# Kernel optimization log

Hardware: AMD Instinct MI355X
Metric: run time of the kernel (lower is better)

The kernel has to match this reference:

```python
import jax, jax.numpy as jnp
import numpy as np

BN_EPS = 1e-5


def _binary_activation(x):
    # forward value = sign(x); gradient flows through piecewise poly o3 (STE)
    s = jnp.sign(x)
    o1 = jnp.where(x < -1.0, -1.0, x * x + 2.0 * x)
    o2 = jnp.where(x < 0.0, o1, -x * x + 2.0 * x)
    o3 = jnp.where(x < 1.0, o2, 1.0)
    return jax.lax.stop_gradient(s - o3) + o3


def _binarize_weights(w):
    # sign_function: fwd 2*(w>0)-1, bwd identity (STE)
    sgn = 2.0 * (w > 0.0).astype(w.dtype) - 1.0
    wb = jax.lax.stop_gradient(sgn - w) + w
    # detached per-output-channel scale: mean |w| over (in, kh, kw)
    scale = jax.lax.stop_gradient(jnp.mean(jnp.abs(w), axis=(1, 2, 3), keepdims=True))
    return scale * wb


def setup_inputs() -> dict:
    key = jax.random.key(0)
    k1, k2, k3 = jax.random.split(key, 3)
    C = 64
    x = jax.random.normal(k1, (32, C, 112, 112), dtype=jnp.float32)
    w = jax.random.uniform(k2, (C, C, 3, 3), dtype=jnp.float32) * 0.001
    return {
        "x": x,
        "b0": jnp.zeros((1, C, 1, 1), jnp.float32),
        "w": w,
        "gamma": jnp.ones((C,), jnp.float32),
        "beta": jnp.zeros((C,), jnp.float32),
        "b1": jnp.zeros((1, C, 1, 1), jnp.float32),
        "alpha": jnp.full((C,), 0.25, jnp.float32),  # PReLU default init
        "b2": jnp.zeros((1, C, 1, 1), jnp.float32),
    }


def reference(x, b0, w, gamma, beta, b1, alpha, b2):
    residual = x
    out = x + b0                       # move0
    out = _binary_activation(out)      # binary activation
    bw = _binarize_weights(w)
    out = jax.lax.conv_general_dilated(
        out, bw, window_strides=(1, 1), padding=[(1, 1), (1, 1)],
        dimension_numbers=("NCHW", "OIHW", "NCHW"))
    # BatchNorm2d in training mode (batch stats, biased variance)
    mu = jnp.mean(out, axis=(0, 2, 3), keepdims=True)
    var = jnp.var(out, axis=(0, 2, 3), keepdims=True)
    g = gamma.reshape(1, -1, 1, 1)
    b = beta.reshape(1, -1, 1, 1)
    out = (out - mu) * jax.lax.rsqrt(var + BN_EPS) * g + b
    out = out + residual
    out = out + b1                     # move1
    a = alpha.reshape(1, -1, 1, 1)
    out = jnp.where(out > 0, out, a * out)  # PReLU
    out = out + b2                     # move2
    return out
```

## Files before the change

### kernel.cpp

```cpp
#include <hip/hip_runtime.h>
#include <stdint.h>

#define C 64
#define HH 112
#define WWD 112
#define HW 12544
#define NB 32
#define MTOT (NB*HW)
#define PLANE_SH 25088
#define PLANE_BYTES 50176
#define ROWB 7168
#define HOLE_OFF 25088

typedef int v4i  __attribute__((ext_vector_type(4)));
typedef int v16i __attribute__((ext_vector_type(16)));
typedef unsigned long long ull;

__device__ __forceinline__ const char* sign_row_c(const char* outb, int R) {
    return outb + (size_t)(R/3)*PLANE_BYTES + HOLE_OFF + (size_t)(R%3)*ROWB;
}
__device__ __forceinline__ char* sign_row(char* outb, int R) {
    return outb + (size_t)(R/3)*PLANE_BYTES + HOLE_OFF + (size_t)(R%3)*ROWB;
}

__global__ __launch_bounds__(256) void k_pack(
        const float* __restrict__ x, const float* __restrict__ b0,
        const float* __restrict__ w,
        char* __restrict__ outb, char* __restrict__ A8, float* __restrict__ wscale) {
    int bid = blockIdx.x;
    if (bid < 1568) {
        __shared__ ull Tl[256*9];
        int tid = threadIdx.x;
        int n    = bid / 49;
        int pimg = (bid % 49) * 256 + tid;
        const float* xb = x + (size_t)n*C*HW + pimg;
        ull row[8];
        #pragma unroll
        for (int k = 0; k < 8; ++k) {
            ull r = 0;
            #pragma unroll
            for (int j = 0; j < 8; ++j) {
                int c = k*8 + j;
                float v = xb[(size_t)c*HW] + b0[c];
                int sg = v > 0.f ? 1 : (v < 0.f ? 0xFF : 0);
                r |= ((ull)(unsigned)sg) << (8*j);
            }
            row[k] = r;
        }
        #pragma unroll
        for (int k = 0; k < 8; ++k) Tl[tid*9 + k] = row[k];
        __syncthreads();
        int wv = tid >> 6, L = tid & 63;
        #pragma unroll
        for (int j = 0; j < 4; ++j) {
            int prow = wv*64 + j*16 + (L >> 2);
            int cch  = L & 3;
            ull a0 = Tl[prow*9 + cch*2];
            ull a1 = Tl[prow*9 + cch*2 + 1];
            int pb = (bid % 49)*256 + wv*64 + j*16;
            int hg = pb / WWD;
            int wg = pb - hg*WWD;
            char* dst = sign_row(outb, n*HH + hg) + wg*64 + (size_t)L*16;
            uint4 val;
            val.x = (uint32_t)a0; val.y = (uint32_t)(a0 >> 32);
            val.z = (uint32_t)a1; val.w = (uint32_t)(a1 >> 32);
            *(uint4*)dst = val;
        }
    } else {
        int t = threadIdx.x;
        int o = t >> 2, part = t & 3;
        float s = 0.f;
        for (int cc = 0; cc < 16; ++cc) {
            int c = part*16 + cc;
            const float* wp = w + ((size_t)o*C + c)*9;
            #pragma unroll
            for (int tap = 0; tap < 9; ++tap) {
                float v = wp[tap];
                s += fabsf(v);
                A8[(o*9 + tap)*64 + c] = v > 0.f ? (char)1 : (char)-1;
            }
        }
        __shared__ float pabs[256];
        pabs[t] = s;
        __syncthreads();
        if (t < 64)
            wscale[t] = (pabs[t*4]+pabs[t*4+1]+pabs[t*4+2]+pabs[t*4+3]) * (1.0f/576.0f);
    }
}

__global__ __launch_bounds__(256) void k_conv(
        const char* __restrict__ signb, const char* __restrict__ A8,
        short* __restrict__ cv16) {
    __shared__ ull ldsq[4*114*9];
    int n  = blockIdx.y;
    int rb = blockIdx.x * 2;

    for (int it = threadIdx.x; it < 4*448; it += 256) {
        int ri = it / 448;
        int k  = it - ri*448;
        int col = k >> 2;
        int b   = k & 3;
        int Rr = rb - 1 + ri;
        uint4 v = make_uint4(0,0,0,0);
        if (Rr >= 0 && Rr < HH)
            v = ((const uint4*)sign_row_c(signb, n*HH + Rr))[k];
        ull* d = &ldsq[((size_t)(ri*114 + col + 1))*9 + b*2];
        d[0] = ((ull)v.y << 32) | v.x;
        d[1] = ((ull)v.w << 32) | v.z;
    }
    if (threadIdx.x < 72) {
        int r = threadIdx.x / 18, rest = threadIdx.x % 18;
        int col = (rest / 9) * 113, q = rest % 9;
        ldsq[((size_t)(r*114 + col))*9 + q] = 0ull;
    }

    int lane  = threadIdx.x & 63;
    int wv    = threadIdx.x >> 6;
    int ot    = wv & 1;
    int gsel  = lane >> 5;
    int olane = ot*32 + (lane & 31);

    v4i afr[9][2];
    #pragma unroll
    for (int tap = 0; tap < 9; ++tap) {
        #pragma unroll
        for (int h = 0; h < 2; ++h)
            afr[tap][h] = *(const v4i*)(A8 + (size_t)(olane*9 + tap)*64 + h*32 + gsel*16);
    }
    __syncthreads();

    for (int T = (wv >> 1); T < 7; T += 2) {
        int px   = T*32 + (lane & 31);
        int roff = px >= WWD ? 1 : 0;
        int cpx  = px - roff*WWD;
        v16i accA = {0,0,0,0,0,0,0,0,0,0,0,0,0,0,0,0};
        v16i accB = {0,0,0,0,0,0,0,0,0,0,0,0,0,0,0,0};
        #pragma unroll
        for (int kh = 0; kh < 3; ++kh) {
            #pragma unroll
            for (int kw = 0; kw < 3; ++kw) {
                const ull* bp = &ldsq[((size_t)((roff+kh)*114 + (cpx+kw)))*9];
                ull lo0 = bp[gsel*2],     hi0 = bp[gsel*2 + 1];
                ull lo1 = bp[gsel*2 + 4], hi1 = bp[gsel*2 + 5];
                v4i b0v = {(int)lo0, (int)(lo0>>32), (int)hi0, (int)(hi0>>32)};
                v4i b1v = {(int)lo1, (int)(lo1>>32), (int)hi1, (int)(hi1>>32)};
                accA = __builtin_amdgcn_mfma_i32_32x32x32_i8(afr[kh*3+kw][0], b0v, accA, 0, 0, 0);
                accB = __builtin_amdgcn_mfma_i32_32x32x32_i8(afr[kh*3+kw][1], b1v, accB, 0, 0, 0);
            }
        }
        v16i acc = accA + accB;
        size_t pixbase = (size_t)rb*WWD + px;
        #pragma unroll
        for (int r = 0; r < 16; ++r) {
            int o = ot*32 + (r & 3) + 8*(r >> 2) + 4*gsel;
            cv16[(size_t)(n*C + o)*PLANE_SH + pixbase] = (short)acc[r];
        }
    }
}

__global__ __launch_bounds__(256) void k_stats(
        const short* __restrict__ cv16, int* __restrict__ ps,
        long long* __restrict__ pq) {
    int plane = blockIdx.x;
    const uint2* p = (const uint2*)(cv16 + (size_t)plane*PLANE_SH);
    int s = 0; unsigned q = 0;
    for (int i = threadIdx.x; i < 3136; i += 256) {
        uint2 u = p[i];
        int v0 = (int)(short)(u.x & 0xFFFF), v1 = (int)(short)(u.x >> 16);
        int v2 = (int)(short)(u.y & 0xFFFF), v3 = (int)(short)(u.y >> 16);
        s += (v0+v1) + (v2+v3);
        q += (unsigned)(v0*v0 + v1*v1) + (unsigned)(v2*v2 + v3*v3);
    }
    __shared__ int ls[256];
    __shared__ unsigned long long lq[256];
    ls[threadIdx.x] = s; lq[threadIdx.x] = q;
    __syncthreads();
    for (int st = 128; st > 0; st >>= 1) {
        if ((int)threadIdx.x < st) {
            ls[threadIdx.x] += ls[threadIdx.x+st];
            lq[threadIdx.x] += lq[threadIdx.x+st];
        }
        __syncthreads();
    }
    if (threadIdx.x == 0) { ps[plane] = ls[0]; pq[plane] = (long long)lq[0]; }
}

__global__ __launch_bounds__(256) void k_finish(
        const short* __restrict__ cv16, const float* __restrict__ x,
        const int* __restrict__ ps, const long long* __restrict__ pq,
        const float* __restrict__ wscale, const float* __restrict__ gamma,
        const float* __restrict__ beta, const float* __restrict__ b1,
        const float* __restrict__ alpha, const float* __restrict__ b2,
        float* __restrict__ out) {
    int o = blockIdx.x, n = blockIdx.y;
    size_t plane = (size_t)n*C + o;

    int s = 0; long long q = 0;
    #pragma unroll 8
    for (int nn = 0; nn < NB; ++nn) { s += ps[nn*C + o]; q += pq[nn*C + o]; }
    const float inv = 1.0f / (float)MTOT;
    float sc   = wscale[o];
    float mean = (float)s * inv;
    float ek2  = (float)q * inv;
    float mu   = sc * mean;
    float var  = sc*sc*ek2 - mu*mu;
    float g    = gamma[o] * rsqrtf(var + 1e-5f);
    float A    = g * sc;
    float B    = beta[o] - g*mu + b1[o];
    float al   = alpha[o];
    float bb2  = b2[o];

    const uint2* cv2 = (const uint2*)(cv16 + plane*PLANE_SH);
    uint2 rbuf[13];
    #pragma unroll
    for (int k = 0; k < 13; ++k) {
        int i = threadIdx.x + k*256;
        if (i < 3136) rbuf[k] = cv2[i];
    }
    __syncthreads();

    const float4* x4 = (const float4*)x + plane*3136;
    float4*       o4 = (float4*)out     + plane*3136;
    #pragma unroll
    for (int k = 0; k < 13; ++k) {
        int i = threadIdx.x + k*256;
        if (i < 3136) {
            uint2 u = rbuf[k];
            float4 xv = x4[i], r;
            float t;
            t = A * (float)(int)(short)(u.x & 0xFFFF) + B + xv.x; t = t > 0.f ? t : al*t; r.x = t + bb2;
            t = A * (float)(int)(short)(u.x >> 16)    + B + xv.y; t = t > 0.f ? t : al*t; r.y = t + bb2;
            t = A * (float)(int)(short)(u.y & 0xFFFF) + B + xv.z; t = t > 0.f ? t : al*t; r.z = t + bb2;
            t = A * (float)(int)(short)(u.y >> 16)    + B + xv.w; t = t > 0.f ? t : al*t; r.w = t + bb2;
            o4[i] = r;
        }
    }
}

extern "C" void kernel_launch(void* const* d_in, const int* in_sizes, int n_in,
                              void* d_out, int out_size, void* d_ws, size_t ws_size,
                              hipStream_t stream) {
    const float* x     = (const float*)d_in[0];
    const float* b0    = (const float*)d_in[1];
    const float* w     = (const float*)d_in[2];
    const float* gamma = (const float*)d_in[3];
    const float* beta  = (const float*)d_in[4];
    const float* b1    = (const float*)d_in[5];
    const float* alpha = (const float*)d_in[6];
    const float* b2    = (const float*)d_in[7];

    char* ws = (char*)d_ws;
    char*      A8     = ws;
    float*     wscale = (float*)(ws + 36864);
    int*       ps     = (int*)(ws + 37120);
    long long* pq     = (long long*)(ws + 45312);

    char*  outb = (char*)d_out;
    short* cv16 = (short*)d_out;

    hipLaunchKernelGGL(k_pack, dim3(1569), dim3(256), 0, stream,
                       x, b0, w, outb, A8, wscale);
    hipLaunchKernelGGL(k_conv, dim3(56, 32), dim3(256), 0, stream,
                       outb, A8, cv16);
    hipLaunchKernelGGL(k_stats, dim3(2048), dim3(256), 0, stream,
                       cv16, ps, pq);
    hipLaunchKernelGGL(k_finish, dim3(64, 32), dim3(256), 0, stream,
                       cv16, x, ps, pq, wscale, gamma, beta, b1, alpha, b2,
                       (float*)d_out);
}
```

Baseline: 120.5 us.

## Fuse activation sign-packing into conv kernel, drop packed intermediate buffer

Removes the separate pack pass that wrote channel-interleaved sign bytes into the output buffer. The conv kernel now reads fp32 x rows directly, computes sign bytes, and transposes them to channel-minor layout with lane shuffles and byte permutes before storing to LDS. Weight prep moves to its own single-block kernel. This avoids a global write and read of the packed sign tensor and one pass over it. In exchange, each input row is loaded as fp32 by two neighbouring row-blocks (halo rows), and the conv prologue does more ALU and shuffle work.

```diff
diff --git a/kernel.cpp b/kernel.cpp
--- a/kernel.cpp
+++ b/kernel.cpp
@@ -8,115 +8,87 @@
 #define NB 32
 #define MTOT (NB*HW)
 #define PLANE_SH 25088
-#define PLANE_BYTES 50176
-#define ROWB 7168
-#define HOLE_OFF 25088
 
 typedef int v4i  __attribute__((ext_vector_type(4)));
 typedef int v16i __attribute__((ext_vector_type(16)));
 typedef unsigned long long ull;
 
-__device__ __forceinline__ const char* sign_row_c(const char* outb, int R) {
-    return outb + (size_t)(R/3)*PLANE_BYTES + HOLE_OFF + (size_t)(R%3)*ROWB;
-}
-__device__ __forceinline__ char* sign_row(char* outb, int R) {
-    return outb + (size_t)(R/3)*PLANE_BYTES + HOLE_OFF + (size_t)(R%3)*ROWB;
-}
-
-__global__ __launch_bounds__(256) void k_pack(
+__device__ __forceinline__ uint32_t sgn_byte(float v) {
+    return v > 0.f ? 1u : (v < 0.f ? 0xFFu : 0u);
+}
+
+__global__ __launch_bounds__(256) void k_wprep(
+        const float* __restrict__ w, char* __restrict__ A8,
+        float* __restrict__ wscale) {
+    int t = threadIdx.x;
+    int o = t >> 2, part = t & 3;
+    float s = 0.f;
+    for (int cc = 0; cc < 16; ++cc) {
+        int c = part*16 + cc;
+        const float* wp = w + ((size_t)o*C + c)*9;
+        #pragma unroll
+        for (int tap = 0; tap < 9; ++tap) {
+            float v = wp[tap];
+            s += fabsf(v);
+            A8[(o*9 + tap)*64 + c] = v > 0.f ? (char)1 : (char)-1;
+        }
+    }
+    __shared__ float pabs[256];
+    pabs[t] = s;
+    __syncthreads();
+    if (t < 64)
+        wscale[t] = (pabs[t*4]+pabs[t*4+1]+pabs[t*4+2]+pabs[t*4+3]) * (1.0f/576.0f);
+}
+
+__global__ __launch_bounds__(256) void k_conv(
         const float* __restrict__ x, const float* __restrict__ b0,
-        const float* __restrict__ w,
-        char* __restrict__ outb, char* __restrict__ A8, float* __restrict__ wscale) {
-    int bid = blockIdx.x;
-    if (bid < 1568) {
-        __shared__ ull Tl[256*9];
-        int tid = threadIdx.x;
-        int n    = bid / 49;
-        int pimg = (bid % 49) * 256 + tid;
-        const float* xb = x + (size_t)n*C*HW + pimg;
-        ull row[8];
-        #pragma unroll
-        for (int k = 0; k < 8; ++k) {
-            ull r = 0;
-            #pragma unroll
-            for (int j = 0; j < 8; ++j) {
-                int c = k*8 + j;
-                float v = xb[(size_t)c*HW] + b0[c];
-                int sg = v > 0.f ? 1 : (v < 0.f ? 0xFF : 0);
-                r |= ((ull)(unsigned)sg) << (8*j);
-            }
-            row[k] = r;
-        }
-        #pragma unroll
-        for (int k = 0; k < 8; ++k) Tl[tid*9 + k] = row[k];
-        __syncthreads();
-        int wv = tid >> 6, L = tid & 63;
-        #pragma unroll
-        for (int j = 0; j < 4; ++j) {
-            int prow = wv*64 + j*16 + (L >> 2);
-            int cch  = L & 3;
-            ull a0 = Tl[prow*9 + cch*2];
-            ull a1 = Tl[prow*9 + cch*2 + 1];
-            int pb = (bid % 49)*256 + wv*64 + j*16;
-            int hg = pb / WWD;
-            int wg = pb - hg*WWD;
-            char* dst = sign_row(outb, n*HH + hg) + wg*64 + (size_t)L*16;
-            uint4 val;
-            val.x = (uint32_t)a0; val.y = (uint32_t)(a0 >> 32);
-            val.z = (uint32_t)a1; val.w = (uint32_t)(a1 >> 32);
-            *(uint4*)dst = val;
-        }
-    } else {
-        int t = threadIdx.x;
-        int o = t >> 2, part = t & 3;
-        float s = 0.f;
-        for (int cc = 0; cc < 16; ++cc) {
-            int c = part*16 + cc;
-            const float* wp = w + ((size_t)o*C + c)*9;
-            #pragma unroll
-            for (int tap = 0; tap < 9; ++tap) {
-                float v = wp[tap];
-                s += fabsf(v);
-                A8[(o*9 + tap)*64 + c] = v > 0.f ? (char)1 : (char)-1;
-            }
-        }
-        __shared__ float pabs[256];
-        pabs[t] = s;
-        __syncthreads();
-        if (t < 64)
-            wscale[t] = (pabs[t*4]+pabs[t*4+1]+pabs[t*4+2]+pabs[t*4+3]) * (1.0f/576.0f);
-    }
-}
-
-__global__ __launch_bounds__(256) void k_conv(
-        const char* __restrict__ signb, const char* __restrict__ A8,
-        short* __restrict__ cv16) {
+        const char* __restrict__ A8, short* __restrict__ cv16) {
     __shared__ ull ldsq[4*114*9];
+    char* ldsb = (char*)ldsq;
     int n  = blockIdx.y;
     int rb = blockIdx.x * 2;
 
-    for (int it = threadIdx.x; it < 4*448; it += 256) {
-        int ri = it / 448;
-        int k  = it - ri*448;
-        int col = k >> 2;
-        int b   = k & 3;
-        int Rr = rb - 1 + ri;
-        uint4 v = make_uint4(0,0,0,0);
-        if (Rr >= 0 && Rr < HH)
-            v = ((const uint4*)sign_row_c(signb, n*HH + Rr))[k];
-        ull* d = &ldsq[((size_t)(ri*114 + col + 1))*9 + b*2];
-        d[0] = ((ull)v.y << 32) | v.x;
-        d[1] = ((ull)v.w << 32) | v.z;
-    }
+    int wv = threadIdx.x >> 6;
+    int L  = threadIdx.x & 63;
+    int Rr = rb - 1 + wv;
+    float bc = b0[L];
+
     if (threadIdx.x < 72) {
         int r = threadIdx.x / 18, rest = threadIdx.x % 18;
         int col = (rest / 9) * 113, q = rest % 9;
-        ldsq[((size_t)(r*114 + col))*9 + q] = 0ull;
+        ldsq[(size_t)(r*114 + col)*9 + q] = 0ull;
+    }
+
+    int k = L & 3, g = L >> 2;
+    uint32_t sel1 = (k & 1) ? 0x07030501u : 0x02060004u;
+    uint32_t sel2 = (k & 2) ? 0x07060302u : 0x01000504u;
+
+    if (Rr >= 0 && Rr < HH) {
+        const float4* src = (const float4*)(x + (size_t)n*C*HW + (size_t)L*HW
+                                              + (size_t)Rr*WWD);
+        #pragma unroll
+        for (int j = 0; j < 28; ++j) {
+            float4 v = src[j];
+            uint32_t d = sgn_byte(v.x + bc)        | (sgn_byte(v.y + bc) << 8)
+                       | (sgn_byte(v.z + bc) << 16) | (sgn_byte(v.w + bc) << 24);
+            uint32_t e  = (uint32_t)__shfl_xor((int)d, 1);
+            uint32_t r1 = __builtin_amdgcn_perm(d, e, sel1);
+            uint32_t f  = (uint32_t)__shfl_xor((int)r1, 2);
+            uint32_t r2 = __builtin_amdgcn_perm(r1, f, sel2);
+            int col = 4*j + k;
+            *(uint32_t*)&ldsb[(size_t)(wv*114 + col + 1)*72 + g*4] = r2;
+        }
+    } else {
+        #pragma unroll
+        for (int j = 0; j < 28; ++j) {
+            int col = 4*j + k;
+            *(uint32_t*)&ldsb[(size_t)(wv*114 + col + 1)*72 + g*4] = 0u;
+        }
     }
 
     int lane  = threadIdx.x & 63;
-    int wv    = threadIdx.x >> 6;
-    int ot    = wv & 1;
+    int wvi   = threadIdx.x >> 6;
+    int ot    = wvi & 1;
     int gsel  = lane >> 5;
     int olane = ot*32 + (lane & 31);
 
@@ -129,7 +101,7 @@
     }
     __syncthreads();
 
-    for (int T = (wv >> 1); T < 7; T += 2) {
+    for (int T = (wvi >> 1); T < 7; T += 2) {
         int px   = T*32 + (lane & 31);
         int roff = px >= WWD ? 1 : 0;
         int cpx  = px - roff*WWD;
@@ -255,13 +227,11 @@
     int*       ps     = (int*)(ws + 37120);
     long long* pq     = (long long*)(ws + 45312);
 
-    char*  outb = (char*)d_out;
     short* cv16 = (short*)d_out;
 
-    hipLaunchKernelGGL(k_pack, dim3(1569), dim3(256), 0, stream,
-                       x, b0, w, outb, A8, wscale);
+    hipLaunchKernelGGL(k_wprep, dim3(1), dim3(256), 0, stream, w, A8, wscale);
     hipLaunchKernelGGL(k_conv, dim3(56, 32), dim3(256), 0, stream,
-                       outb, A8, cv16);
+                       x, b0, A8, cv16);
     hipLaunchKernelGGL(k_stats, dim3(2048), dim3(256), 0, stream,
                        cv16, ps, pq);
     hipLaunchKernelGGL(k_finish, dim3(64, 32), dim3(256), 0, stream,
```

After: 140.0 us. +16.1%, slower.
